# Kernel optimization log

Measured on AMD Instinct MI355X. Metric: run time of the kernel, lower is better.

Reference implementation:

```python
import jax, jax.numpy as jnp
import numpy as np

P, F, V = 2048, 8192, 2048


def setup_inputs() -> dict:
    key = jax.random.key(0)
    k1, k2, k3 = jax.random.split(key, 3)
    points = jax.random.normal(k1, (P, 3), dtype=jnp.float32)
    vertices = jax.random.normal(k2, (V, 3), dtype=jnp.float32)
    faces = jax.random.randint(k3, (F, 3), 0, V, dtype=jnp.int32)
    return {"points": points, "vertices": vertices, "faces": faces}


def _triangle_weights(points, a, b, c):
    """Barycentric weights of closest point on each triangle (a,b,c) [F,3]
    for each point [P,3], via Ericson's region classification.
    All pairwise dot products expanded so only [P,F] scalars are materialized
    (never [P,F,3] differences)."""
    ab = b - a  # [F,3]
    ac = c - a  # [F,3]
    pab = points @ ab.T  # [P,F] = dot(p, ab)
    pac = points @ ac.T  # [P,F] = dot(p, ac)
    d1 = pab - jnp.sum(a * ab, -1)  # dot(ab, p-a)
    d2 = pac - jnp.sum(a * ac, -1)  # dot(ac, p-a)
    d3 = pab - jnp.sum(b * ab, -1)  # dot(ab, p-b)
    d4 = pac - jnp.sum(b * ac, -1)  # dot(ac, p-b)
    d5 = pab - jnp.sum(c * ab, -1)  # dot(ab, p-c)
    d6 = pac - jnp.sum(c * ac, -1)  # dot(ac, p-c)
    vc = d1 * d4 - d3 * d2
    vb = d5 * d2 - d1 * d6
    va = d3 * d6 - d5 * d4

    def sdiv(n, d):
        ds = jnp.where(d == 0, 1.0, d)
        return n / ds

    # region 7 (interior) is the default; overwrite with higher-priority
    denom = va + vb + vc
    v7 = sdiv(vb, denom)
    w7 = sdiv(vc, denom)
    w1, w2, w3 = 1.0 - v7 - w7, v7, w7
    # region 6: edge bc
    t6 = sdiv(d4 - d3, (d4 - d3) + (d5 - d6))
    m6 = (va <= 0) & (d4 - d3 >= 0) & (d5 - d6 >= 0)
    w1 = jnp.where(m6, 0.0, w1)
    w2 = jnp.where(m6, 1.0 - t6, w2)
    w3 = jnp.where(m6, t6, w3)
    # region 5: edge ac
    t5 = sdiv(d2, d2 - d6)
    m5 = (vb <= 0) & (d2 >= 0) & (d6 <= 0)
    w1 = jnp.where(m5, 1.0 - t5, w1)
    w2 = jnp.where(m5, 0.0, w2)
    w3 = jnp.where(m5, t5, w3)
    # region 4: vertex c
    m4 = (d6 >= 0) & (d5 <= d6)
    w1 = jnp.where(m4, 0.0, w1)
    w2 = jnp.where(m4, 0.0, w2)
    w3 = jnp.where(m4, 1.0, w3)
    # region 3: edge ab
    t3 = sdiv(d1, d1 - d3)
    m3 = (vc <= 0) & (d1 >= 0) & (d3 <= 0)
    w1 = jnp.where(m3, 1.0 - t3, w1)
    w2 = jnp.where(m3, t3, w2)
    w3 = jnp.where(m3, 0.0, w3)
    # region 2: vertex b
    m2 = (d3 >= 0) & (d4 <= d3)
    w1 = jnp.where(m2, 0.0, w1)
    w2 = jnp.where(m2, 1.0, w2)
    w3 = jnp.where(m2, 0.0, w3)
    # region 1: vertex a
    m1 = (d1 <= 0) & (d2 <= 0)
    w1 = jnp.where(m1, 1.0, w1)
    w2 = jnp.where(m1, 0.0, w2)
    w3 = jnp.where(m1, 0.0, w3)
    return w1, w2, w3  # each [P,F]


def reference(points, vertices, faces):
    # gather per-face vertex triples (the f1/f2/f3 of the torch module)
    a = vertices[faces[:, 0]]  # [F,3]
    b = vertices[faces[:, 1]]
    c = vertices[faces[:, 2]]
    w1, w2, w3 = _triangle_weights(points, a, b, c)  # [P,F] each
    cp = w1[..., None] * a + w2[..., None] * b + w3[..., None] * c  # [P,F,3]
    dist = jnp.sum((points[:, None, :] - cp) ** 2, axis=-1)  # [P,F]
    idx = jnp.argmin(dist, axis=1)  # [P] closest face per point
    gather = lambda w: jnp.take_along_axis(w, idx[:, None], axis=1)[:, 0]
    return idx, gather(w1), gather(w2), gather(w3)
```

## Files before the change

### kernel.cpp

```cpp
#include <hip/hip_runtime.h>
#include <cstdint>

#pragma clang fp contract(off)

typedef float v2f __attribute__((ext_vector_type(2)));

#define P_N 2048
#define F_N 8192
#define V_N 2048

#define TPB 256
#define FACES_PER_TILE 32

__device__ __forceinline__ void face_setup(
    const float* __restrict__ vertices, const int* __restrict__ faces, int f,
    float* fd)
{
#pragma clang fp contract(off)
    int i0 = faces[3 * f + 0];
    int i1 = faces[3 * f + 1];
    int i2 = faces[3 * f + 2];
    float ax = vertices[3 * i0 + 0], ay = vertices[3 * i0 + 1], az = vertices[3 * i0 + 2];
    float bx = vertices[3 * i1 + 0], by = vertices[3 * i1 + 1], bz = vertices[3 * i1 + 2];
    float cx = vertices[3 * i2 + 0], cy = vertices[3 * i2 + 1], cz = vertices[3 * i2 + 2];
    float abx = bx - ax, aby = by - ay, abz = bz - az;
    float acx = cx - ax, acy = cy - ay, acz = cz - az;
    float daab = (ax * abx + ay * aby) + az * abz;
    float daac = (ax * acx + ay * acy) + az * acz;
    float dbab = (bx * abx + by * aby) + bz * abz;
    float dbac = (bx * acx + by * acy) + bz * acz;
    float dcab = (cx * abx + cy * aby) + cz * abz;
    float dcac = (cx * acx + cy * acy) + cz * acz;
    fd[0] = ax;  fd[1] = ay;  fd[2] = az;
    fd[3] = bx;  fd[4] = by;  fd[5] = bz;
    fd[6] = cx;  fd[7] = cy;  fd[8] = cz;
    fd[9] = abx; fd[10] = aby; fd[11] = abz;
    fd[12] = acx; fd[13] = acy; fd[14] = acz;
    fd[15] = daab; fd[16] = daac; fd[17] = dbab;
    fd[18] = dbac; fd[19] = dcab; fd[20] = dcac;
}

__device__ __forceinline__ void region_w(
    float d1, float d2, float d3, float d4, float d5, float d6,
    float va, float vb, float vc, float e63, float e65, float denom,
    float& w1, float& w2, float& w3)
{
#pragma clang fp contract(off)
    bool m1 = (d1 <= 0.0f) & (d2 <= 0.0f);
    bool m2 = (d3 >= 0.0f) & (d4 <= d3);
    bool m3 = (vc <= 0.0f) & (d1 >= 0.0f) & (d3 <= 0.0f);
    bool m4 = (d6 >= 0.0f) & (d5 <= d6);
    bool m5 = (vb <= 0.0f) & (d2 >= 0.0f) & (d6 <= 0.0f);
    bool m6 = (va <= 0.0f) & (e63 >= 0.0f) & (e65 >= 0.0f);
    bool anym = m1 | m2 | m3 | m4 | m5 | m6;

    float n1  = m1 ? 0.0f : m2 ? 0.0f : m3 ? d1          : m4 ? 0.0f : m5 ? d2          : m6 ? e63         : vb;
    float ds1 = m1 ? 1.0f : m2 ? 1.0f : m3 ? (d1 - d3)   : m4 ? 1.0f : m5 ? (d2 - d6)   : m6 ? (e63 + e65) : denom;
    ds1 = (ds1 == 0.0f) ? 1.0f : ds1;
    float n2  = anym ? 0.0f : vc;
    float ds2 = anym ? 1.0f : ((denom == 0.0f) ? 1.0f : denom);

    float q1 = n1 / ds1;
    float q2 = n2 / ds2;
    float u = (1.0f - q1) - q2;

    w1 = m1 ? 1.0f : m2 ? 0.0f : m3 ? u    : m4 ? 0.0f : m5 ? u    : m6 ? 0.0f : u;
    w2 = m1 ? 0.0f : m2 ? 1.0f : m3 ? q1   : m4 ? 0.0f : m5 ? 0.0f : m6 ? u    : q1;
    w3 = m1 ? 0.0f : m2 ? 0.0f : m3 ? 0.0f : m4 ? 1.0f : m5 ? q1   : m6 ? q1   : q2;
}

__device__ __forceinline__ void tri_eval_exact(
    float px, float py, float pz,
    const float* fd,
    float& w1o, float& w2o, float& w3o, float& disto)
{
#pragma clang fp contract(off)
    const float ax = fd[0], ay = fd[1], az = fd[2];
    const float bx = fd[3], by = fd[4], bz = fd[5];
    const float cx = fd[6], cy = fd[7], cz = fd[8];
    const float abx = fd[9], aby = fd[10], abz = fd[11];
    const float acx = fd[12], acy = fd[13], acz = fd[14];
    const float daab = fd[15], daac = fd[16], dbab = fd[17];
    const float dbac = fd[18], dcab = fd[19], dcac = fd[20];

    float pab = fmaf(pz, abz, fmaf(py, aby, px * abx));
    float pac = fmaf(pz, acz, fmaf(py, acy, px * acx));

    float d1 = pab - daab;
    float d2 = pac - daac;
    float d3 = pab - dbab;
    float d4 = pac - dbac;
    float d5 = pab - dcab;
    float d6 = pac - dcac;

    float vc = d1 * d4 - d3 * d2;
    float vb = d5 * d2 - d1 * d6;
    float va = d3 * d6 - d5 * d4;

    float denom = (va + vb) + vc;
    float dn = (denom == 0.0f) ? 1.0f : denom;
    float v7 = vb / dn;
    float w7 = vc / dn;
    float w1 = (1.0f - v7) - w7;
    float w2 = v7;
    float w3 = w7;

    float e63 = d4 - d3;
    float e65 = d5 - d6;
    float t6d = e63 + e65; t6d = (t6d == 0.0f) ? 1.0f : t6d;
    float t6 = e63 / t6d;
    if ((va <= 0.0f) & (e63 >= 0.0f) & (e65 >= 0.0f)) { w1 = 0.0f; w2 = 1.0f - t6; w3 = t6; }

    float t5d = d2 - d6; t5d = (t5d == 0.0f) ? 1.0f : t5d;
    float t5 = d2 / t5d;
    if ((vb <= 0.0f) & (d2 >= 0.0f) & (d6 <= 0.0f)) { w1 = 1.0f - t5; w2 = 0.0f; w3 = t5; }

    if ((d6 >= 0.0f) & (d5 <= d6)) { w1 = 0.0f; w2 = 0.0f; w3 = 1.0f; }

    float t3d = d1 - d3; t3d = (t3d == 0.0f) ? 1.0f : t3d;
    float t3 = d1 / t3d;
    if ((vc <= 0.0f) & (d1 >= 0.0f) & (d3 <= 0.0f)) { w1 = 1.0f - t3; w2 = t3; w3 = 0.0f; }

    if ((d3 >= 0.0f) & (d4 <= d3)) { w1 = 0.0f; w2 = 1.0f; w3 = 0.0f; }

    if ((d1 <= 0.0f) & (d2 <= 0.0f)) { w1 = 1.0f; w2 = 0.0f; w3 = 0.0f; }

    float cpx = (w1 * ax + w2 * bx) + w3 * cx;
    float cpy = (w1 * ay + w2 * by) + w3 * cy;
    float cpz = (w1 * az + w2 * bz) + w3 * cz;
    float dx = px - cpx, dy = py - cpy, dz = pz - cpz;
    float dist = (dx * dx + dy * dy) + dz * dz;

    w1o = w1; w2o = w2; w3o = w3; disto = dist;
}

__global__ __launch_bounds__(TPB) void k_scan(
    const float* __restrict__ points,
    const float* __restrict__ vertices,
    const int* __restrict__ faces,
    unsigned long long* __restrict__ best)
{
#pragma clang fp contract(off)
    __shared__ float sq[21][FACES_PER_TILE];

    const int pblk = blockIdx.x;
    const int fblk = blockIdx.y;
    const int t = threadIdx.x;

    if (t < FACES_PER_TILE) {
        int f = fblk * FACES_PER_TILE + t;
        float fd[21];
        face_setup(vertices, faces, f, fd);
#pragma unroll
        for (int k = 0; k < 21; ++k) sq[k][t] = fd[k];
    }
    __syncthreads();

    const int p = pblk * TPB + t;
    const float px = points[3 * p + 0];
    const float py = points[3 * p + 1];
    const float pz = points[3 * p + 2];
    const v2f pxv = {px, px};
    const v2f pyv = {py, py};
    const v2f pzv = {pz, pz};

    unsigned int bestdb = 0xffffffffu;
    int bestf = 0;
    const int fbase = fblk * FACES_PER_TILE;

#pragma unroll 2
    for (int j = 0; j < FACES_PER_TILE; j += 2) {
#define LD2(q) (*(const v2f*)&sq[q][j])
        v2f axv = LD2(0),  ayv = LD2(1),  azv = LD2(2);
        v2f bxv = LD2(3),  byv = LD2(4),  bzv = LD2(5);
        v2f cxv = LD2(6),  cyv = LD2(7),  czv = LD2(8);
        v2f abxv = LD2(9),  abyv = LD2(10), abzv = LD2(11);
        v2f acxv = LD2(12), acyv = LD2(13), aczv = LD2(14);
        v2f daabv = LD2(15), daacv = LD2(16), dbabv = LD2(17);
        v2f dbacv = LD2(18), dcabv = LD2(19), dcacv = LD2(20);
#undef LD2

        v2f pab = __builtin_elementwise_fma(pzv, abzv,
                    __builtin_elementwise_fma(pyv, abyv, pxv * abxv));
        v2f pac = __builtin_elementwise_fma(pzv, aczv,
                    __builtin_elementwise_fma(pyv, acyv, pxv * acxv));

        v2f d1 = pab - daabv;
        v2f d2 = pac - daacv;
        v2f d3 = pab - dbabv;
        v2f d4 = pac - dbacv;
        v2f d5 = pab - dcabv;
        v2f d6 = pac - dcacv;

        v2f vcv = d1 * d4 - d3 * d2;
        v2f vbv = d5 * d2 - d1 * d6;
        v2f vav = d3 * d6 - d5 * d4;

        v2f e63 = d4 - d3;
        v2f e65 = d5 - d6;
        v2f denom = (vav + vbv) + vcv;

        float w1a, w2a, w3a, w1b, w2b, w3b;
        region_w(d1.x, d2.x, d3.x, d4.x, d5.x, d6.x,
                 vav.x, vbv.x, vcv.x, e63.x, e65.x, denom.x, w1a, w2a, w3a);
        region_w(d1.y, d2.y, d3.y, d4.y, d5.y, d6.y,
                 vav.y, vbv.y, vcv.y, e63.y, e65.y, denom.y, w1b, w2b, w3b);

        v2f w1v = {w1a, w1b};
        v2f w2v = {w2a, w2b};
        v2f w3v = {w3a, w3b};

        v2f cpx = (w1v * axv + w2v * bxv) + w3v * cxv;
        v2f cpy = (w1v * ayv + w2v * byv) + w3v * cyv;
        v2f cpz = (w1v * azv + w2v * bzv) + w3v * czv;
        v2f dx = pxv - cpx, dy = pyv - cpy, dz = pzv - cpz;
        v2f dist = (dx * dx + dy * dy) + dz * dz;

        float da = dist.x;
        float db = dist.y;
        unsigned int ua = __float_as_uint(da);
        unsigned int ub = __float_as_uint(db);
        if (da != da) ua = 0u;
        if (db != db) ub = 0u;
        if (ua < bestdb) { bestdb = ua; bestf = fbase + j; }
        if (ub < bestdb) { bestdb = ub; bestf = fbase + j + 1; }
    }

    unsigned long long key =
        ((unsigned long long)bestdb << 32) | (unsigned int)bestf;
    atomicMin(&best[p], key);
}

__global__ __launch_bounds__(TPB) void k_final(
    const float* __restrict__ points,
    const float* __restrict__ vertices,
    const int* __restrict__ faces,
    const unsigned long long* __restrict__ best,
    float* __restrict__ out)
{
    const int p = blockIdx.x * TPB + threadIdx.x;
    if (p >= P_N) return;
    unsigned long long bk = best[p];
    int f = (int)(bk & 0xffffffffull);

    float fd[21];
    face_setup(vertices, faces, f, fd);

    const float px = points[3 * p + 0];
    const float py = points[3 * p + 1];
    const float pz = points[3 * p + 2];
    float w1, w2, w3, dist;
    tri_eval_exact(px, py, pz, fd, w1, w2, w3, dist);

    out[p] = (float)f;
    out[P_N + p] = w1;
    out[2 * P_N + p] = w2;
    out[3 * P_N + p] = w3;
}

extern "C" void kernel_launch(void* const* d_in, const int* in_sizes, int n_in,
                              void* d_out, int out_size, void* d_ws, size_t ws_size,
                              hipStream_t stream)
{
    const float* points = (const float*)d_in[0];
    const float* vertices = (const float*)d_in[1];
    const int* faces = (const int*)d_in[2];
    float* out = (float*)d_out;
    unsigned long long* best = (unsigned long long*)d_ws;

    hipMemsetAsync(d_ws, 0xFF, P_N * sizeof(unsigned long long), stream);

    dim3 grid(P_N / TPB, F_N / FACES_PER_TILE);
    k_scan<<<grid, TPB, 0, stream>>>(points, vertices, faces, best);
    k_final<<<(P_N + TPB - 1) / TPB, TPB, 0, stream>>>(points, vertices, faces, best, out);
}
```

Before: 55.95 us.

## Prune faces with plane-distance lower bound against per-point upper bound

Adds a prep kernel that precomputes a per-face table holding setup data plus the plane normal, offset and inverse squared normal length. A bound kernel then evaluates one exact distance per face tile to set a per-point upper bound. The scan kernel skips the full closest-point evaluation for a face whenever no lane in the wave has a plane-distance lower bound under its threshold. This trades two extra launches and scalar, non-packed evaluation for possible skipped work, but wave-wide voting and large random triangles may leave little to prune.

```diff
diff --git a/kernel.cpp b/kernel.cpp
--- a/kernel.cpp
+++ b/kernel.cpp
@@ -7,10 +7,16 @@
 
 #define P_N 2048
 #define F_N 8192
-#define V_N 2048
-
 #define TPB 256
-#define FACES_PER_TILE 32
+#define FPT 32
+#define NT (F_N / FPT)
+#define TW 28
+
+#define WS_TAB_BYTES   (F_N * TW * 4)
+#define WS_MINUB_OFF   WS_TAB_BYTES
+#define WS_BEST_OFF    (WS_TAB_BYTES + P_N * 4)
+#define WS_NEEDED      (WS_BEST_OFF + P_N * 8)
+
 
 __device__ __forceinline__ void face_setup(
     const float* __restrict__ vertices, const int* __restrict__ faces, int f,
@@ -40,6 +46,208 @@
     fd[18] = dbac; fd[19] = dcab; fd[20] = dcac;
 }
 
+__device__ __forceinline__ void tri_eval_exact(
+    float px, float py, float pz,
+    const float* __restrict__ fd,
+    float& w1o, float& w2o, float& w3o, float& disto)
+{
+#pragma clang fp contract(off)
+    const float ax = fd[0], ay = fd[1], az = fd[2];
+    const float bx = fd[3], by = fd[4], bz = fd[5];
+    const float cx = fd[6], cy = fd[7], cz = fd[8];
+    const float abx = fd[9], aby = fd[10], abz = fd[11];
+    const float acx = fd[12], acy = fd[13], acz = fd[14];
+    const float daab = fd[15], daac = fd[16], dbab = fd[17];
+    const float dbac = fd[18], dcab = fd[19], dcac = fd[20];
+
+    float pab = fmaf(pz, abz, fmaf(py, aby, px * abx));
+    float pac = fmaf(pz, acz, fmaf(py, acy, px * acx));
+
+    float d1 = pab - daab;
+    float d2 = pac - daac;
+    float d3 = pab - dbab;
+    float d4 = pac - dbac;
+    float d5 = pab - dcab;
+    float d6 = pac - dcac;
+
+    float vc = d1 * d4 - d3 * d2;
+    float vb = d5 * d2 - d1 * d6;
+    float va = d3 * d6 - d5 * d4;
+
+    float denom = (va + vb) + vc;
+    float dn = (denom == 0.0f) ? 1.0f : denom;
+    float v7 = vb / dn;
+    float w7 = vc / dn;
+    float w1 = (1.0f - v7) - w7;
+    float w2 = v7;
+    float w3 = w7;
+
+    float e63 = d4 - d3;
+    float e65 = d5 - d6;
+    float t6d = e63 + e65; t6d = (t6d == 0.0f) ? 1.0f : t6d;
+    float t6 = e63 / t6d;
+    if ((va <= 0.0f) & (e63 >= 0.0f) & (e65 >= 0.0f)) { w1 = 0.0f; w2 = 1.0f - t6; w3 = t6; }
+
+    float t5d = d2 - d6; t5d = (t5d == 0.0f) ? 1.0f : t5d;
+    float t5 = d2 / t5d;
+    if ((vb <= 0.0f) & (d2 >= 0.0f) & (d6 <= 0.0f)) { w1 = 1.0f - t5; w2 = 0.0f; w3 = t5; }
+
+    if ((d6 >= 0.0f) & (d5 <= d6)) { w1 = 0.0f; w2 = 0.0f; w3 = 1.0f; }
+
+    float t3d = d1 - d3; t3d = (t3d == 0.0f) ? 1.0f : t3d;
+    float t3 = d1 / t3d;
+    if ((vc <= 0.0f) & (d1 >= 0.0f) & (d3 <= 0.0f)) { w1 = 1.0f - t3; w2 = t3; w3 = 0.0f; }
+
+    if ((d3 >= 0.0f) & (d4 <= d3)) { w1 = 0.0f; w2 = 1.0f; w3 = 0.0f; }
+
+    if ((d1 <= 0.0f) & (d2 <= 0.0f)) { w1 = 1.0f; w2 = 0.0f; w3 = 0.0f; }
+
+    float cpx = (w1 * ax + w2 * bx) + w3 * cx;
+    float cpy = (w1 * ay + w2 * by) + w3 * cy;
+    float cpz = (w1 * az + w2 * bz) + w3 * cz;
+    float dx = px - cpx, dy = py - cpy, dz = pz - cpz;
+    float dist = (dx * dx + dy * dy) + dz * dz;
+
+    w1o = w1; w2o = w2; w3o = w3; disto = dist;
+}
+
+
+__global__ __launch_bounds__(TPB) void k_prep(
+    const float* __restrict__ vertices, const int* __restrict__ faces,
+    float* __restrict__ tab, unsigned* __restrict__ minub,
+    unsigned long long* __restrict__ best)
+{
+#pragma clang fp contract(off)
+    int f = blockIdx.x * TPB + threadIdx.x;
+    if (f < F_N) {
+        float td[TW];
+        face_setup(vertices, faces, f, td);
+        float ax = td[0], ay = td[1], az = td[2];
+        float abx = td[9], aby = td[10], abz = td[11];
+        float acx = td[12], acy = td[13], acz = td[14];
+        float nx = aby * acz - abz * acy;
+        float ny = abz * acx - abx * acz;
+        float nz = abx * acy - aby * acx;
+        float nn = (nx * nx + ny * ny) + nz * nz;
+        float abab = (abx * abx + aby * aby) + abz * abz;
+        float acac = (acx * acx + acy * acy) + acz * acz;
+        float L2v = abab + acac;
+        bool bad = !(nn >= 1e-2f * L2v) || (nn < 1e-20f);
+        td[21] = nx; td[22] = ny; td[23] = nz;
+        td[24] = -((nx * ax + ny * ay) + nz * az);
+        td[25] = bad ? -1.0f : 1.0f / nn;
+        td[26] = 0.0f; td[27] = 0.0f;
+#pragma unroll
+        for (int k = 0; k < TW; k += 4)
+            *(float4*)&tab[f * TW + k] = *(float4*)&td[k];
+    }
+    if (f < P_N) {
+        minub[f] = 0x7f7f7f7fu;
+        best[f] = ~0ull;
+    }
+}
+
+
+__global__ __launch_bounds__(TPB) void k_bound(
+    const float* __restrict__ points,
+    const float* __restrict__ tab,
+    unsigned* __restrict__ minub)
+{
+#pragma clang fp contract(off)
+    const int pblk = blockIdx.x, fblk = blockIdx.y, t = threadIdx.x;
+    const int fbase = fblk * FPT;
+    const int p = pblk * TPB + t;
+    const float px = points[3 * p + 0];
+    const float py = points[3 * p + 1];
+    const float pz = points[3 * p + 2];
+
+    float bestv = 1e30f;
+    int bestj = fbase;
+
+#pragma unroll 4
+    for (int j = 0; j < FPT; ++j) {
+        const float* __restrict__ tf = tab + (size_t)(fbase + j) * TW;
+        float nx = tf[21], ny = tf[22], nz = tf[23], mnd = tf[24], inn = tf[25];
+        float nd = fmaf(nz, pz, fmaf(ny, py, fmaf(nx, px, mnd)));
+        float p2 = (nd * nd) * inn;
+        bool better = (p2 >= 0.0f) & (p2 < bestv);
+        bestv = better ? p2 : bestv;
+        bestj = better ? (fbase + j) : bestj;
+    }
+
+    float fd[21];
+#pragma unroll
+    for (int k = 0; k < 20; k += 4)
+        *(float4*)&fd[k] = *(const float4*)&tab[(size_t)bestj * TW + k];
+    fd[20] = tab[(size_t)bestj * TW + 20];
+    float w1, w2, w3, dist;
+    tri_eval_exact(px, py, pz, fd, w1, w2, w3, dist);
+    if (!(dist != dist)) atomicMin(&minub[p], __float_as_uint(dist));
+}
+
+
+__global__ __launch_bounds__(TPB) void k_scan2(
+    const float* __restrict__ points,
+    const float* __restrict__ tab,
+    const unsigned* __restrict__ minub,
+    unsigned long long* __restrict__ best)
+{
+#pragma clang fp contract(off)
+    const int pblk = blockIdx.x, fblk = blockIdx.y, t = threadIdx.x;
+    const int fbase = fblk * FPT;
+    const int p = pblk * TPB + t;
+    const float px = points[3 * p + 0];
+    const float py = points[3 * p + 1];
+    const float pz = points[3 * p + 2];
+    const float thr = __uint_as_float(minub[p]);
+
+    unsigned bestdb = 0xffffffffu;
+    int bestf = 0;
+
+#pragma unroll 2
+    for (int j = 0; j < FPT; ++j) {
+        const float* __restrict__ tf = tab + (size_t)(fbase + j) * TW;
+        float nx = tf[21], ny = tf[22], nz = tf[23], mnd = tf[24], inn = tf[25];
+        float nd = fmaf(nz, pz, fmaf(ny, py, fmaf(nx, px, mnd)));
+        float p2 = (nd * nd) * inn;
+        float lb = fmaxf(fmaf(p2, 0.97f, -1e-6f), 0.0f);
+        if (__any(lb <= thr)) {
+            float w1, w2, w3, dist;
+            tri_eval_exact(px, py, pz, tf, w1, w2, w3, dist);
+            unsigned db = __float_as_uint(dist);
+            if (dist != dist) db = 0u;
+            if (db < bestdb) { bestdb = db; bestf = fbase + j; }
+        }
+    }
+
+    unsigned long long key =
+        ((unsigned long long)bestdb << 32) | (unsigned)bestf;
+    atomicMin(&best[p], key);
+}
+
+
+__global__ __launch_bounds__(TPB) void k_final(
+    const float* __restrict__ points,
+    const float* __restrict__ vertices,
+    const int* __restrict__ faces,
+    const unsigned long long* __restrict__ best,
+    float* __restrict__ out)
+{
+    const int p = blockIdx.x * TPB + threadIdx.x;
+    if (p >= P_N) return;
+    int f = (int)(best[p] & 0x1fffull);
+    float fd[21];
+    face_setup(vertices, faces, f, fd);
+    float w1, w2, w3, dist;
+    tri_eval_exact(points[3 * p], points[3 * p + 1], points[3 * p + 2],
+                   fd, w1, w2, w3, dist);
+    out[p] = (float)f;
+    out[P_N + p] = w1;
+    out[2 * P_N + p] = w2;
+    out[3 * P_N + p] = w3;
+}
+
+
 __device__ __forceinline__ void region_w(
     float d1, float d2, float d3, float d4, float d5, float d6,
     float va, float vb, float vc, float e63, float e65, float denom,
@@ -54,8 +262,8 @@
     bool m6 = (va <= 0.0f) & (e63 >= 0.0f) & (e65 >= 0.0f);
     bool anym = m1 | m2 | m3 | m4 | m5 | m6;
 
-    float n1  = m1 ? 0.0f : m2 ? 0.0f : m3 ? d1          : m4 ? 0.0f : m5 ? d2          : m6 ? e63         : vb;
-    float ds1 = m1 ? 1.0f : m2 ? 1.0f : m3 ? (d1 - d3)   : m4 ? 1.0f : m5 ? (d2 - d6)   : m6 ? (e63 + e65) : denom;
+    float n1  = m1 ? 0.0f : m2 ? 0.0f : m3 ? d1        : m4 ? 0.0f : m5 ? d2        : m6 ? e63         : vb;
+    float ds1 = m1 ? 1.0f : m2 ? 1.0f : m3 ? (d1 - d3) : m4 ? 1.0f : m5 ? (d2 - d6) : m6 ? (e63 + e65) : denom;
     ds1 = (ds1 == 0.0f) ? 1.0f : ds1;
     float n2  = anym ? 0.0f : vc;
     float ds2 = anym ? 1.0f : ((denom == 0.0f) ? 1.0f : denom);
@@ -69,107 +277,33 @@
     w3 = m1 ? 0.0f : m2 ? 0.0f : m3 ? 0.0f : m4 ? 1.0f : m5 ? q1   : m6 ? q1   : q2;
 }
 
-__device__ __forceinline__ void tri_eval_exact(
-    float px, float py, float pz,
-    const float* fd,
-    float& w1o, float& w2o, float& w3o, float& disto)
-{
-#pragma clang fp contract(off)
-    const float ax = fd[0], ay = fd[1], az = fd[2];
-    const float bx = fd[3], by = fd[4], bz = fd[5];
-    const float cx = fd[6], cy = fd[7], cz = fd[8];
-    const float abx = fd[9], aby = fd[10], abz = fd[11];
-    const float acx = fd[12], acy = fd[13], acz = fd[14];
-    const float daab = fd[15], daac = fd[16], dbab = fd[17];
-    const float dbac = fd[18], dcab = fd[19], dcac = fd[20];
-
-    float pab = fmaf(pz, abz, fmaf(py, aby, px * abx));
-    float pac = fmaf(pz, acz, fmaf(py, acy, px * acx));
-
-    float d1 = pab - daab;
-    float d2 = pac - daac;
-    float d3 = pab - dbab;
-    float d4 = pac - dbac;
-    float d5 = pab - dcab;
-    float d6 = pac - dcac;
-
-    float vc = d1 * d4 - d3 * d2;
-    float vb = d5 * d2 - d1 * d6;
-    float va = d3 * d6 - d5 * d4;
-
-    float denom = (va + vb) + vc;
-    float dn = (denom == 0.0f) ? 1.0f : denom;
-    float v7 = vb / dn;
-    float w7 = vc / dn;
-    float w1 = (1.0f - v7) - w7;
-    float w2 = v7;
-    float w3 = w7;
-
-    float e63 = d4 - d3;
-    float e65 = d5 - d6;
-    float t6d = e63 + e65; t6d = (t6d == 0.0f) ? 1.0f : t6d;
-    float t6 = e63 / t6d;
-    if ((va <= 0.0f) & (e63 >= 0.0f) & (e65 >= 0.0f)) { w1 = 0.0f; w2 = 1.0f - t6; w3 = t6; }
-
-    float t5d = d2 - d6; t5d = (t5d == 0.0f) ? 1.0f : t5d;
-    float t5 = d2 / t5d;
-    if ((vb <= 0.0f) & (d2 >= 0.0f) & (d6 <= 0.0f)) { w1 = 1.0f - t5; w2 = 0.0f; w3 = t5; }
-
-    if ((d6 >= 0.0f) & (d5 <= d6)) { w1 = 0.0f; w2 = 0.0f; w3 = 1.0f; }
-
-    float t3d = d1 - d3; t3d = (t3d == 0.0f) ? 1.0f : t3d;
-    float t3 = d1 / t3d;
-    if ((vc <= 0.0f) & (d1 >= 0.0f) & (d3 <= 0.0f)) { w1 = 1.0f - t3; w2 = t3; w3 = 0.0f; }
-
-    if ((d3 >= 0.0f) & (d4 <= d3)) { w1 = 0.0f; w2 = 1.0f; w3 = 0.0f; }
-
-    if ((d1 <= 0.0f) & (d2 <= 0.0f)) { w1 = 1.0f; w2 = 0.0f; w3 = 0.0f; }
-
-    float cpx = (w1 * ax + w2 * bx) + w3 * cx;
-    float cpy = (w1 * ay + w2 * by) + w3 * cy;
-    float cpz = (w1 * az + w2 * bz) + w3 * cz;
-    float dx = px - cpx, dy = py - cpy, dz = pz - cpz;
-    float dist = (dx * dx + dy * dy) + dz * dz;
-
-    w1o = w1; w2o = w2; w3o = w3; disto = dist;
-}
-
-__global__ __launch_bounds__(TPB) void k_scan(
+__global__ __launch_bounds__(TPB) void k_scan_full(
     const float* __restrict__ points,
     const float* __restrict__ vertices,
     const int* __restrict__ faces,
     unsigned long long* __restrict__ best)
 {
 #pragma clang fp contract(off)
-    __shared__ float sq[21][FACES_PER_TILE];
-
-    const int pblk = blockIdx.x;
-    const int fblk = blockIdx.y;
-    const int t = threadIdx.x;
-
-    if (t < FACES_PER_TILE) {
-        int f = fblk * FACES_PER_TILE + t;
+    __shared__ float sq[21][FPT];
+    const int pblk = blockIdx.x, fblk = blockIdx.y, t = threadIdx.x;
+    if (t < FPT) {
         float fd[21];
-        face_setup(vertices, faces, f, fd);
+        face_setup(vertices, faces, fblk * FPT + t, fd);
 #pragma unroll
         for (int k = 0; k < 21; ++k) sq[k][t] = fd[k];
     }
     __syncthreads();
 
     const int p = pblk * TPB + t;
-    const float px = points[3 * p + 0];
-    const float py = points[3 * p + 1];
-    const float pz = points[3 * p + 2];
-    const v2f pxv = {px, px};
-    const v2f pyv = {py, py};
-    const v2f pzv = {pz, pz};
+    const float px = points[3 * p], py = points[3 * p + 1], pz = points[3 * p + 2];
+    const v2f pxv = {px, px}, pyv = {py, py}, pzv = {pz, pz};
 
     unsigned int bestdb = 0xffffffffu;
     int bestf = 0;
-    const int fbase = fblk * FACES_PER_TILE;
+    const int fbase = fblk * FPT;
 
 #pragma unroll 2
-    for (int j = 0; j < FACES_PER_TILE; j += 2) {
+    for (int j = 0; j < FPT; j += 2) {
 #define LD2(q) (*(const v2f*)&sq[q][j])
         v2f axv = LD2(0),  ayv = LD2(1),  azv = LD2(2);
         v2f bxv = LD2(3),  byv = LD2(4),  bzv = LD2(5);
@@ -179,25 +313,16 @@
         v2f daabv = LD2(15), daacv = LD2(16), dbabv = LD2(17);
         v2f dbacv = LD2(18), dcabv = LD2(19), dcacv = LD2(20);
 #undef LD2
-
         v2f pab = __builtin_elementwise_fma(pzv, abzv,
                     __builtin_elementwise_fma(pyv, abyv, pxv * abxv));
         v2f pac = __builtin_elementwise_fma(pzv, aczv,
                     __builtin_elementwise_fma(pyv, acyv, pxv * acxv));
-
-        v2f d1 = pab - daabv;
-        v2f d2 = pac - daacv;
-        v2f d3 = pab - dbabv;
-        v2f d4 = pac - dbacv;
-        v2f d5 = pab - dcabv;
-        v2f d6 = pac - dcacv;
-
+        v2f d1 = pab - daabv, d2 = pac - daacv, d3 = pab - dbabv;
+        v2f d4 = pac - dbacv, d5 = pab - dcabv, d6 = pac - dcacv;
         v2f vcv = d1 * d4 - d3 * d2;
         v2f vbv = d5 * d2 - d1 * d6;
         v2f vav = d3 * d6 - d5 * d4;
-
-        v2f e63 = d4 - d3;
-        v2f e65 = d5 - d6;
+        v2f e63 = d4 - d3, e65 = d5 - d6;
         v2f denom = (vav + vbv) + vcv;
 
         float w1a, w2a, w3a, w1b, w2b, w3b;
@@ -206,20 +331,15 @@
         region_w(d1.y, d2.y, d3.y, d4.y, d5.y, d6.y,
                  vav.y, vbv.y, vcv.y, e63.y, e65.y, denom.y, w1b, w2b, w3b);
 
-        v2f w1v = {w1a, w1b};
-        v2f w2v = {w2a, w2b};
-        v2f w3v = {w3a, w3b};
-
+        v2f w1v = {w1a, w1b}, w2v = {w2a, w2b}, w3v = {w3a, w3b};
         v2f cpx = (w1v * axv + w2v * bxv) + w3v * cxv;
         v2f cpy = (w1v * ayv + w2v * byv) + w3v * cyv;
         v2f cpz = (w1v * azv + w2v * bzv) + w3v * czv;
         v2f dx = pxv - cpx, dy = pyv - cpy, dz = pzv - cpz;
         v2f dist = (dx * dx + dy * dy) + dz * dz;
 
-        float da = dist.x;
-        float db = dist.y;
-        unsigned int ua = __float_as_uint(da);
-        unsigned int ub = __float_as_uint(db);
+        float da = dist.x, db = dist.y;
+        unsigned ua = __float_as_uint(da), ub = __float_as_uint(db);
         if (da != da) ua = 0u;
         if (db != db) ub = 0u;
         if (ua < bestdb) { bestdb = ua; bestf = fbase + j; }
@@ -231,33 +351,6 @@
     atomicMin(&best[p], key);
 }
 
-__global__ __launch_bounds__(TPB) void k_final(
-    const float* __restrict__ points,
-    const float* __restrict__ vertices,
-    const int* __restrict__ faces,
-    const unsigned long long* __restrict__ best,
-    float* __restrict__ out)
-{
-    const int p = blockIdx.x * TPB + threadIdx.x;
-    if (p >= P_N) return;
-    unsigned long long bk = best[p];
-    int f = (int)(bk & 0xffffffffull);
-
-    float fd[21];
-    face_setup(vertices, faces, f, fd);
-
-    const float px = points[3 * p + 0];
-    const float py = points[3 * p + 1];
-    const float pz = points[3 * p + 2];
-    float w1, w2, w3, dist;
-    tri_eval_exact(px, py, pz, fd, w1, w2, w3, dist);
-
-    out[p] = (float)f;
-    out[P_N + p] = w1;
-    out[2 * P_N + p] = w2;
-    out[3 * P_N + p] = w3;
-}
-
 extern "C" void kernel_launch(void* const* d_in, const int* in_sizes, int n_in,
                               void* d_out, int out_size, void* d_ws, size_t ws_size,
                               hipStream_t stream)
@@ -266,11 +359,21 @@
     const float* vertices = (const float*)d_in[1];
     const int* faces = (const int*)d_in[2];
     float* out = (float*)d_out;
-    unsigned long long* best = (unsigned long long*)d_ws;
-
-    hipMemsetAsync(d_ws, 0xFF, P_N * sizeof(unsigned long long), stream);
-
-    dim3 grid(P_N / TPB, F_N / FACES_PER_TILE);
-    k_scan<<<grid, TPB, 0, stream>>>(points, vertices, faces, best);
-    k_final<<<(P_N + TPB - 1) / TPB, TPB, 0, stream>>>(points, vertices, faces, best, out);
-}
+    char* ws = (char*)d_ws;
+
+    if (ws_size >= WS_NEEDED) {
+        float* tab = (float*)ws;
+        unsigned* minub = (unsigned*)(ws + WS_MINUB_OFF);
+        unsigned long long* best = (unsigned long long*)(ws + WS_BEST_OFF);
+
+        k_prep<<<F_N / TPB, TPB, 0, stream>>>(vertices, faces, tab, minub, best);
+        k_bound<<<dim3(P_N / TPB, NT), TPB, 0, stream>>>(points, tab, minub);
+        k_scan2<<<dim3(P_N / TPB, NT), TPB, 0, stream>>>(points, tab, minub, best);
+        k_final<<<(P_N + TPB - 1) / TPB, TPB, 0, stream>>>(points, vertices, faces, best, out);
+    } else {
+        unsigned long long* best = (unsigned long long*)ws;
+        hipMemsetAsync(best, 0xFF, P_N * sizeof(unsigned long long), stream);
+        k_scan_full<<<dim3(P_N / TPB, NT), TPB, 0, stream>>>(points, vertices, faces, best);
+        k_final<<<(P_N + TPB - 1) / TPB, TPB, 0, stream>>>(points, vertices, faces, best, out);
+    }
+}
```

Result: slower. 66.31 us (+18.5%).
